# Kernel optimization log

Measured on AMD Instinct MI355X. Metric: run time of the kernel, lower is better.

## Reference

```python
import jax, jax.numpy as jnp
import numpy as np

S, M, B, D, H, DH = 1024, 1024, 4, 1024, 16, 64
T = S + M


def _rel_shift(x):
    # x: [i, j, b, n] -> Transformer-XL relative shift
    i, j = x.shape[0], x.shape[1]
    zero_pad = jnp.zeros((i, 1) + x.shape[2:], x.dtype)
    x_padded = jnp.concatenate([zero_pad, x], axis=1)
    x_padded = x_padded.reshape((j + 1, i) + x.shape[2:])
    return x_padded[1:].reshape(x.shape)


def setup_inputs() -> dict:
    key = jax.random.key(0)
    ks = jax.random.split(key, 8)
    sc = 0.02
    x = jax.random.normal(ks[0], (S, B, D), jnp.float32)
    memory = jax.random.normal(ks[1], (M, B, D), jnp.float32)
    pos_emb = jax.random.normal(ks[2], (T, D), jnp.float32)
    pos_bias_u = jax.random.normal(ks[3], (H, DH), jnp.float32) * sc
    pos_bias_v = jax.random.normal(ks[4], (H, DH), jnp.float32) * sc
    W_qkv = jax.random.normal(ks[5], (D, 3 * H * DH), jnp.float32) * sc
    W_rel = jax.random.normal(ks[6], (D, H * DH), jnp.float32) * sc
    W_o = jax.random.normal(ks[7], (H * DH, D), jnp.float32) * sc
    gamma = jnp.ones((D,), jnp.float32)
    beta = jnp.zeros((D,), jnp.float32)
    # causal mask accounting for memory: query i attends keys j <= i + M
    causal = jnp.arange(T)[None, :] > (jnp.arange(S)[:, None] + M)
    mask = jnp.broadcast_to(causal[:, :, None], (S, T, B))
    return {"x": x, "pos_emb": pos_emb, "pos_bias_u": pos_bias_u,
            "pos_bias_v": pos_bias_v, "memory": memory,
            "W_qkv": W_qkv, "W_rel": W_rel, "W_o": W_o,
            "gamma": gamma, "beta": beta, "mask": mask}


def reference(x, pos_emb, pos_bias_u, pos_bias_v, memory, W_qkv, W_rel, W_o, gamma, beta, mask):
    seq_len, batch, d_model = x.shape
    num_head, d_head = pos_bias_u.shape
    scale = 1.0 / d_head ** 0.5

    c = jnp.concatenate([memory, x], axis=0)          # [T, B, D]
    total_len = c.shape[0]

    qkv = c @ W_qkv                                   # [T, B, 3*H*DH]
    q, k, v = jnp.split(qkv, 3, axis=-1)
    q = q.reshape(total_len, batch, num_head, d_head)[-seq_len:]  # [S,B,H,DH]
    k = k.reshape(total_len, batch, num_head, d_head)             # [T,B,H,DH]
    v = v.reshape(total_len, batch, num_head, d_head)             # [T,B,H,DH]
    r = (pos_emb @ W_rel).reshape(total_len, num_head, d_head)    # [T,H,DH]

    AC = jnp.einsum('ibnd,jbnd->ijbn', q + pos_bias_u, k)  # content-content
    BD = jnp.einsum('ibnd,jnd->ijbn', q + pos_bias_v, r)   # content-position
    BD = _rel_shift(BD)

    attn_score = (AC + BD) * scale                    # [S,T,B,H]
    attn_score = jnp.where(mask[:, :, :, None], -jnp.inf, attn_score)
    attn_prob = jax.nn.softmax(attn_score, axis=1)

    attn_vec = jnp.einsum('ijbn,jbnd->ibnd', attn_prob, v)
    attn_vec = attn_vec.reshape(seq_len, batch, num_head * d_head)
    attn_out = attn_vec @ W_o                         # [S,B,D]

    y = x + attn_out
    mu = jnp.mean(y, axis=-1, keepdims=True)
    var = jnp.var(y, axis=-1, keepdims=True)
    return (y - mu) / jnp.sqrt(var + 1e-5) * gamma + beta
```

## Files before the change

kernel.cpp:

```cpp
#include <hip/hip_runtime.h>
#include <math.h>
#include <cstdint>
#include <cstddef>


typedef _Float16 half_t;
typedef _Float16 half8 __attribute__((ext_vector_type(8)));
typedef _Float16 half4v __attribute__((ext_vector_type(4)));
typedef float f32x4 __attribute__((ext_vector_type(4)));

#define S_LEN 1024
#define M_LEN 1024
#define T_LEN 2048
#define BATCH 4
#define NHEAD 16

__device__ inline void async_copy16(const half_t* g, half_t* l) {
  __builtin_amdgcn_global_load_lds(
      (const __attribute__((address_space(1))) void*)g,
      (__attribute__((address_space(3))) void*)l, 16, 0, 0);
}

__global__ __launch_bounds__(256) void k_convert3(const float* __restrict__ mem,
                                                  const float* __restrict__ x,
                                                  const float* __restrict__ pos,
                                                  half_t* __restrict__ cbf,
                                                  half_t* __restrict__ posb) {
  const int i = blockIdx.x * 256 + threadIdx.x;
  const float* src;
  half_t* dst;
  int off;
  if (i < 1048576)      { src = mem; dst = cbf;           off = i; }
  else if (i < 2097152) { src = x;   dst = cbf + 4194304; off = i - 1048576; }
  else                  { src = pos; dst = posb;          off = i - 2097152; }
  const float4 v = ((const float4*)src)[off];
  half4v h;
  h[0] = (half_t)v.x; h[1] = (half_t)v.y; h[2] = (half_t)v.z; h[3] = (half_t)v.w;
  ((half4v*)dst)[off] = h;
}

__global__ __launch_bounds__(256) void k_transpose_w3(const float* __restrict__ Wqkv,
                                                      const float* __restrict__ Wrel,
                                                      const float* __restrict__ Wo,
                                                      half_t* __restrict__ wqkvT,
                                                      half_t* __restrict__ wrelT,
                                                      half_t* __restrict__ woT) {
  __shared__ float tile[64][65];
  const int y = blockIdx.y;
  const float* src; half_t* dst; int C, c0;
  if (y < 48)      { src = Wqkv; dst = wqkvT; C = 3072; c0 = y * 64; }
  else if (y < 64) { src = Wrel; dst = wrelT; C = 1024; c0 = (y - 48) * 64; }
  else             { src = Wo;   dst = woT;   C = 1024; c0 = (y - 64) * 64; }
  const int t = threadIdx.x;
  const int r0 = blockIdx.x * 64;
  const int tx = t & 63, ty4 = t >> 6;
#pragma unroll
  for (int k = 0; k < 16; ++k) {
    int row = k * 4 + ty4;
    tile[row][tx] = src[(size_t)(r0 + row) * C + c0 + tx];
  }
  __syncthreads();
#pragma unroll
  for (int k = 0; k < 16; ++k) {
    int orow = k * 4 + ty4;
    dst[(size_t)(c0 + orow) * 1024 + r0 + tx] = (half_t)tile[tx][orow];
  }
}

__device__ inline void gemm_body(const half_t* __restrict__ A,
                                 const half_t* __restrict__ B,
                                 half_t* __restrict__ C,
                                 int N, int K, int ld, int m0, int n0,
                                 half_t (*ldsA)[64], half_t (*ldsB)[64]) {
  const int t = threadIdx.x;
  const int wave = t >> 6, lane = t & 63, quad = lane >> 4, l15 = lane & 15;
  const int wm = (wave >> 1) * 64, wn = (wave & 1) * 64;
  const int srow = lane >> 3;
  const int scol = ((lane & 7) ^ srow) * 8;
  f32x4 acc[4][4] = {};
  for (int k0 = 0; k0 < K; k0 += 64) {
    __syncthreads();
#pragma unroll
    for (int i = 0; i < 4; ++i) {
      const int r0 = (wave * 4 + i) * 8;
      async_copy16(&A[(size_t)(m0 + r0 + srow) * ld + k0 + scol], &ldsA[r0][0]);
      async_copy16(&B[(size_t)(n0 + r0 + srow) * ld + k0 + scol], &ldsB[r0][0]);
    }
    __syncthreads();
#pragma unroll
    for (int ks = 0; ks < 2; ++ks) {
      half8 af[4], bf[4];
#pragma unroll
      for (int mt = 0; mt < 4; ++mt)
        af[mt] = *(const half8*)&ldsA[wm + mt * 16 + l15][((ks * 4 + quad) ^ (l15 & 7)) * 8];
#pragma unroll
      for (int nt = 0; nt < 4; ++nt)
        bf[nt] = *(const half8*)&ldsB[wn + nt * 16 + l15][((ks * 4 + quad) ^ (l15 & 7)) * 8];
#pragma unroll
      for (int mt = 0; mt < 4; ++mt)
#pragma unroll
        for (int nt = 0; nt < 4; ++nt)
          acc[mt][nt] = __builtin_amdgcn_mfma_f32_16x16x32_f16(af[mt], bf[nt], acc[mt][nt], 0, 0, 0);
    }
  }
#pragma unroll
  for (int mt = 0; mt < 4; ++mt)
#pragma unroll
    for (int nt = 0; nt < 4; ++nt)
#pragma unroll
      for (int r = 0; r < 4; ++r) {
        const int row = m0 + wm + mt * 16 + quad * 4 + r;
        const int col = n0 + wn + nt * 16 + l15;
        C[(size_t)row * N + col] = (half_t)acc[mt][nt][r];
      }
}

#define QP_STAGE(buf_, k0_)                                                    \
  do {                                                                         \
    _Pragma("unroll") for (int i_ = 0; i_ < 4; ++i_) {                         \
      const int r0_ = wave * 32 + i_ * 8;                                      \
      async_copy16(&A[(size_t)(m0 + r0_ + srw) * 1024 + (k0_) + scl],          \
                   &ldsA[buf_][r0_][0]);                                       \
      async_copy16(&B[(size_t)(n0 + r0_ + srw) * 1024 + (k0_) + scl],          \
                   &ldsB[buf_][r0_][0]);                                       \
    }                                                                          \
  } while (0)

#define QP_COMPUTE(d_)                                                         \
  do {                                                                         \
    _Pragma("unroll") for (int ks_ = 0; ks_ < 2; ++ks_) {                      \
      half8 bf_[4];                                                            \
      _Pragma("unroll") for (int nt_ = 0; nt_ < 4; ++nt_) {                    \
        const int rw_ = wn + nt_ * 16 + l15;                                   \
        bf_[nt_] =                                                             \
            *(const half8*)&ldsB[d_][rw_][((ks_ * 4 + quad) ^ (rw_ & 7)) * 8]; \
      }                                                                        \
      half8 af_[8];                                                            \
      _Pragma("unroll") for (int mt_ = 0; mt_ < 8; ++mt_) {                    \
        const int rw_ = wm + mt_ * 16 + l15;                                   \
        af_[mt_] =                                                             \
            *(const half8*)&ldsA[d_][rw_][((ks_ * 4 + quad) ^ (rw_ & 7)) * 8]; \
      }                                                                        \
      __builtin_amdgcn_s_setprio(1);                                           \
      _Pragma("unroll") for (int mt_ = 0; mt_ < 8; ++mt_)                      \
        _Pragma("unroll") for (int nt_ = 0; nt_ < 4; ++nt_)                    \
          acc[mt_][nt_] = __builtin_amdgcn_mfma_f32_16x16x32_f16(              \
              af_[mt_], bf_[nt_], acc[mt_][nt_], 0, 0, 0);                     \
      __builtin_amdgcn_s_setprio(0);                                           \
    }                                                                          \
  } while (0)

__global__ __launch_bounds__(512, 2) void k_gemm_qkv_pos(const half_t* __restrict__ cbf,
                                                         const half_t* __restrict__ wqkvT,
                                                         half_t* __restrict__ qkv,
                                                         const half_t* __restrict__ posb,
                                                         const half_t* __restrict__ wrelT,
                                                         half_t* __restrict__ rb) {
  __shared__ half_t ldsA[2][256][64];
  __shared__ half_t ldsB[2][256][64];
  const int t = threadIdx.x;
  const int wave = t >> 6, lane = t & 63, quad = lane >> 4, l15 = lane & 15;
  const int bid0 = blockIdx.x;
  const int bid = (bid0 & 7) * 52 + (bid0 >> 3);
  const half_t* A; const half_t* B; half_t* C; int m0, n0, N;
  if (bid < 384) { A = cbf;  B = wqkvT; C = qkv; N = 3072;
                   m0 = (bid & 31) * 256; n0 = (bid >> 5) * 256; }
  else { const int b2 = bid - 384;
         A = posb; B = wrelT; C = rb;  N = 1024;
         m0 = (b2 & 7) * 256; n0 = (b2 >> 3) * 256; }
  const int srw = lane >> 3;
  const int scl = ((lane & 7) ^ srw) * 8;
  const int wm = (wave >> 2) * 128, wn = (wave & 3) * 64;

  f32x4 acc[8][4] = {};

  QP_STAGE(0, 0);
  __syncthreads();
  int d = 0;
  for (int kt = 0; kt < 15; ++kt) {
    QP_STAGE(d ^ 1, (kt + 1) * 64);
    QP_COMPUTE(d);
    __syncthreads();
    d ^= 1;
  }
  QP_COMPUTE(d);

#pragma unroll
  for (int mt = 0; mt < 8; ++mt)
#pragma unroll
    for (int nt = 0; nt < 4; ++nt)
#pragma unroll
      for (int r = 0; r < 4; ++r)
        C[(size_t)(m0 + wm + mt * 16 + quad * 4 + r) * N + n0 + wn + nt * 16 + l15] =
            (half_t)acc[mt][nt][r];
}

__global__ __launch_bounds__(256) void k_gemm_proj(const half_t* __restrict__ av,
                                                   const half_t* __restrict__ woT,
                                                   half_t* __restrict__ out0,
                                                   half_t* __restrict__ out1) {
  __shared__ half_t ldsA[128][64];
  __shared__ half_t ldsB[128][64];
  const int bid = blockIdx.x;
  const int h = bid >> 8, b2 = bid & 255;
  gemm_body(av + h * 512, woT + h * 512, h ? out1 : out0,
            1024, 512, 1024, (b2 & 31) * 128, (b2 >> 5) * 128, ldsA, ldsB);
}

__global__ __launch_bounds__(256) void k_transpose_v(const half_t* __restrict__ qkv,
                                                     half_t* __restrict__ vT) {
  __shared__ half_t tile[64][72];
  const int t = threadIdx.x;
  const int t0 = blockIdx.x * 64, bn = blockIdx.y, b = bn >> 4, n = bn & 15;
#pragma unroll
  for (int i = 0; i < 2; ++i) {
    const int ci = t + i * 256;
    const int row = ci >> 3, co = (ci & 7) * 8;
    *(half8*)&tile[row][co] =
        *(const half8*)&qkv[((size_t)(t0 + row) * BATCH + b) * 3072 + 2048 + n * 64 + co];
  }
  __syncthreads();
#pragma unroll
  for (int i = 0; i < 2; ++i) {
    const int ci = t + i * 256;
    const int dh = ci >> 3, to = (ci & 7) * 8;
    half8 v;
#pragma unroll
    for (int j = 0; j < 8; ++j) v[j] = tile[to + j][dh];
    *(half8*)&vT[((size_t)bn * 64 + dh) * 2048 + t0 + to] = v;
  }
}

__global__ __launch_bounds__(512, 4) void k_attn(const half_t* __restrict__ qkv,
                                                 const half_t* __restrict__ rbuf,
                                                 const half_t* __restrict__ vT,
                                                 const float* __restrict__ pbu,
                                                 const float* __restrict__ pbv,
                                                 half_t* __restrict__ av) {
  __shared__ __align__(16) half_t ldsK[64][64];
  __shared__ __align__(16) half_t ldsV[64][64];
  __shared__ __align__(16) half_t ldsR[256][64];
  __shared__ __align__(16) half_t ldsP[8][16][72];
  const int t = threadIdx.x;
  const int wave = t >> 6, lane = t & 63, quad = lane >> 4, l15 = lane & 15;

  const int li = blockIdx.x + 8 * blockIdx.y;
  const int c = li & 255, kr = li >> 8;
  const int xe = kr == 0 ? (c & 7) : 7 - (c & 7);
  const int bn = (c >> 3) + (kr << 5);
  const int i0 = xe * 128;
  const int b = bn >> 4, n = bn & 15;
  const int i_base = i0 + wave * 16;
  const int p0 = 896 - i0;

  half8 qu[2], qv[2];
#pragma unroll
  for (int ks = 0; ks < 2; ++ks) {
    const int dh0 = ks * 32 + quad * 8;
    const half8 qf = *(const half8*)&qkv[((size_t)(M_LEN + i_base + l15) * BATCH + b) * 3072 + n * 64 + dh0];
#pragma unroll
    for (int j = 0; j < 8; ++j) {
      const float qj = (float)qf[j];
      qu[ks][j] = (half_t)(qj + pbu[n * 64 + dh0 + j]);
      qv[ks][j] = (half_t)(qj + pbv[n * 64 + dh0 + j]);
    }
  }

  int bperm_idx[4];
  bool lo_sel[4];
#pragma unroll
  for (int r = 0; r < 4; ++r) {
    const int irow = quad * 4 + r;
    bperm_idx[r] = ((lane & 48) | ((l15 + 15 - irow) & 15)) << 2;
    lo_sel[r] = (l15 <= irow);
  }

  f32x4 oacc[4] = {};
  float lpart[4] = {0.f, 0.f, 0.f, 0.f};
  const float k1 = 0.125f * 1.44269504088896f;
  const float kC = -4.0f * 1.44269504088896f;

  const int srow = t >> 3, sc3 = t & 7;
  const int sxk = (sc3 ^ (srow & 7)) * 8;

  const int ntile = xe * 2 + 18;

  half8 kreg = *(const half8*)&qkv[((size_t)srow * BATCH + b) * 3072 + 1024 + n * 64 + sc3 * 8];
  half8 vreg = *(const half8*)&vT[((size_t)bn * 64 + srow) * 2048 + sc3 * 8];
  half8 rreg4[4];
  int rr4[4], rc4[4];
#pragma unroll
  for (int i = 0; i < 4; ++i) {
    const int ci = t + 512 * i;
    rr4[i] = ci >> 3; rc4[i] = ci & 7;
    const int ps = p0 + rr4[i] > 2047 ? 2047 : p0 + rr4[i];
    rreg4[i] = *(const half8*)&rbuf[(size_t)ps * 1024 + n * 64 + rc4[i] * 8];
  }
  half8 rpre;

  for (int kt = 0; kt < ntile; ++kt) {
    const int j0 = kt * 64;

    __syncthreads();
    *(half8*)&ldsK[srow][sxk] = kreg;
    *(half8*)&ldsV[srow][sxk] = vreg;
    if (kt == 0) {
#pragma unroll
      for (int i = 0; i < 4; ++i) {
        const int pg = p0 + rr4[i];
        *(half8*)&ldsR[pg & 255][(rc4[i] ^ (pg & 7)) * 8] = rreg4[i];
      }
    } else {
      const int pw = j0 + p0 + 192 + srow;
      *(half8*)&ldsR[pw & 255][(sc3 ^ (pw & 7)) * 8] = rpre;
    }
    __syncthreads();

    if (kt + 1 < ntile) {
      const int j0n = j0 + 64;
      kreg = *(const half8*)&qkv[((size_t)(j0n + srow) * BATCH + b) * 3072 + 1024 + n * 64 + sc3 * 8];
      vreg = *(const half8*)&vT[((size_t)bn * 64 + srow) * 2048 + j0n + sc3 * 8];
      const int pn = j0 + p0 + 256 + srow;
      const int pc = pn > 2047 ? 2047 : pn;
      rpre = *(const half8*)&rbuf[(size_t)pc * 1024 + n * 64 + sc3 * 8];
    }

    f32x4 ac[4] = {};
#pragma unroll
    for (int ks = 0; ks < 2; ++ks)
#pragma unroll
      for (int nt = 0; nt < 4; ++nt) {
        const int row = nt * 16 + l15;
        const half8 kf = *(const half8*)&ldsK[row][((ks * 4 + quad) ^ (row & 7)) * 8];
        ac[nt] = __builtin_amdgcn_mfma_f32_16x16x32_f16(qu[ks], kf, ac[nt], 0, 0, 0);
      }

    const int rbg = j0 + p0 + 112 - wave * 16;
    f32x4 ea[5] = {};
#pragma unroll
    for (int ks = 0; ks < 2; ++ks)
#pragma unroll
      for (int et = 0; et < 5; ++et) {
        const int pr = rbg + et * 16 + l15;
        const half8 rf = *(const half8*)&ldsR[pr & 255][((ks * 4 + quad) ^ (pr & 7)) * 8];
        ea[et] = __builtin_amdgcn_mfma_f32_16x16x32_f16(qv[ks], rf, ea[et], 0, 0, 0);
      }

    const bool maskt = j0 > i_base + 960;
#pragma unroll
    for (int r = 0; r < 4; ++r) {
      const int irow = quad * 4 + r;
      const int ig = i_base + irow;
      float rot[5];
#pragma unroll
      for (int et = 0; et < 5; ++et)
        rot[et] = __int_as_float(
            __builtin_amdgcn_ds_bpermute(bperm_idx[r], __float_as_int(ea[et][r])));
      float psum = 0.f;
#pragma unroll
      for (int nt = 0; nt < 4; ++nt) {
        const float ev = lo_sel[r] ? rot[nt] : rot[nt + 1];
        const int cj = nt * 16 + l15;
        float p = __builtin_amdgcn_exp2f(fmaf(ac[nt][r] + ev, k1, kC));
        if (maskt && (j0 + cj > ig + M_LEN)) p = 0.f;
        psum += p;
        ldsP[wave][irow][cj] = (half_t)p;
      }
      lpart[r] += psum;
    }
    __builtin_amdgcn_wave_barrier();

    half8 pa[2];
#pragma unroll
    for (int ks = 0; ks < 2; ++ks)
      pa[ks] = *(const half8*)&ldsP[wave][l15][ks * 32 + quad * 8];
#pragma unroll
    for (int ks = 0; ks < 2; ++ks)
#pragma unroll
      for (int dnt = 0; dnt < 4; ++dnt) {
        const int row = dnt * 16 + l15;
        const half8 vf = *(const half8*)&ldsV[row][((ks * 4 + quad) ^ (row & 7)) * 8];
        oacc[dnt] = __builtin_amdgcn_mfma_f32_16x16x32_f16(pa[ks], vf, oacc[dnt], 0, 0, 0);
      }
  }

#pragma unroll
  for (int r = 0; r < 4; ++r) {
    float l = lpart[r];
#pragma unroll
    for (int off = 1; off < 16; off <<= 1) l += __shfl_xor(l, off);
    const float inv = 1.0f / l;
    const int ig = i_base + quad * 4 + r;
#pragma unroll
    for (int dnt = 0; dnt < 4; ++dnt)
      av[((size_t)ig * BATCH + b) * 1024 + n * 64 + dnt * 16 + l15] = (half_t)(oacc[dnt][r] * inv);
  }
}

__global__ __launch_bounds__(256) void k_ln(const float* __restrict__ x,
                                            const half_t* __restrict__ ao0,
                                            const half_t* __restrict__ ao1,
                                            const float* __restrict__ gamma,
                                            const float* __restrict__ beta,
                                            float* __restrict__ out) {
  const int row = blockIdx.x;
  const int t = threadIdx.x;
  const float4 xv = ((const float4*)(x + (size_t)row * 1024))[t];
  const half4v a4 = ((const half4v*)(ao0 + (size_t)row * 1024))[t];
  const half4v b4 = ((const half4v*)(ao1 + (size_t)row * 1024))[t];
  const float y0 = xv.x + (float)a4[0] + (float)b4[0];
  const float y1 = xv.y + (float)a4[1] + (float)b4[1];
  const float y2 = xv.z + (float)a4[2] + (float)b4[2];
  const float y3 = xv.w + (float)a4[3] + (float)b4[3];
  float s = y0 + y1 + y2 + y3;
  float ss = y0 * y0 + y1 * y1 + y2 * y2 + y3 * y3;
#pragma unroll
  for (int off = 1; off < 64; off <<= 1) {
    s += __shfl_xor(s, off);
    ss += __shfl_xor(ss, off);
  }
  __shared__ float sb[4], ssb[4];
  if ((t & 63) == 0) { sb[t >> 6] = s; ssb[t >> 6] = ss; }
  __syncthreads();
  s = sb[0] + sb[1] + sb[2] + sb[3];
  ss = ssb[0] + ssb[1] + ssb[2] + ssb[3];
  const float mean = s * (1.f / 1024.f);
  const float var = ss * (1.f / 1024.f) - mean * mean;
  const float rstd = rsqrtf(var + 1e-5f);
  const float4 g = ((const float4*)gamma)[t];
  const float4 be = ((const float4*)beta)[t];
  float4 o;
  o.x = (y0 - mean) * rstd * g.x + be.x;
  o.y = (y1 - mean) * rstd * g.y + be.y;
  o.z = (y2 - mean) * rstd * g.z + be.z;
  o.w = (y3 - mean) * rstd * g.w + be.w;
  ((float4*)(out + (size_t)row * 1024))[t] = o;
}

extern "C" void kernel_launch(void* const* d_in, const int* in_sizes, int n_in,
                              void* d_out, int out_size, void* d_ws, size_t ws_size,
                              hipStream_t stream) {
  const float* x     = (const float*)d_in[0];
  const float* pos   = (const float*)d_in[1];
  const float* pbu   = (const float*)d_in[2];
  const float* pbv   = (const float*)d_in[3];
  const float* mem   = (const float*)d_in[4];
  const float* Wqkv  = (const float*)d_in[5];
  const float* Wrel  = (const float*)d_in[6];
  const float* Wo    = (const float*)d_in[7];
  const float* gamma = (const float*)d_in[8];
  const float* beta  = (const float*)d_in[9];
  float* out = (float*)d_out;

  half_t* ws    = (half_t*)d_ws;
  half_t* cbf   = ws;
  half_t* posb  = cbf + 8388608;
  half_t* wqkvT = posb + 2097152;
  half_t* wrelT = wqkvT + 3145728;
  half_t* woT   = wrelT + 1048576;
  half_t* qkv   = woT + 1048576;
  half_t* rb    = qkv + 25165824;
  half_t* vT    = rb + 2097152;
  half_t* av    = vT + 8388608;
  half_t* aout0 = qkv;
  half_t* aout1 = qkv + 4194304;

  k_convert3<<<10240, 256, 0, stream>>>(mem, x, pos, cbf, posb);
  k_transpose_w3<<<dim3(16, 80), 256, 0, stream>>>(Wqkv, Wrel, Wo, wqkvT, wrelT, woT);
  k_gemm_qkv_pos<<<416, 512, 0, stream>>>(cbf, wqkvT, qkv, posb, wrelT, rb);
  k_transpose_v<<<dim3(32, 64), 256, 0, stream>>>(qkv, vT);
  k_attn<<<dim3(8, 64), 512, 0, stream>>>(qkv, rb, vT, pbu, pbv, av);
  k_gemm_proj<<<512, 256, 0, stream>>>(av, woT, aout0, aout1);
  k_ln<<<4096, 256, 0, stream>>>(x, aout0, aout1, gamma, beta, out);
}
```

Measured before the change: 330.5 us.

## Compute V transposed directly in GEMM, fuse prep kernels, reorder rows batch-major

Merges the input-conversion and weight-transpose kernels into a single launch. The conversion now writes the concatenated activations batch-major. The QKV GEMM is split so that Q/K go to a narrower buffer. V is produced already transposed by swapping the operands (W_v^T times activations), which removes the separate V-transpose kernel and its round trip through memory. The attention kernel's indexing is updated for the new layouts. The cost is that the V-part blocks write with a large stride (N=8192), and one fewer launch boundary is traded for a more branchy prep kernel.

```diff
diff --git a/kernel.cpp b/kernel.cpp
--- a/kernel.cpp
+++ b/kernel.cpp
@@ -21,38 +21,47 @@
       (__attribute__((address_space(3))) void*)l, 16, 0, 0);
 }
 
-__global__ __launch_bounds__(256) void k_convert3(const float* __restrict__ mem,
-                                                  const float* __restrict__ x,
-                                                  const float* __restrict__ pos,
-                                                  half_t* __restrict__ cbf,
-                                                  half_t* __restrict__ posb) {
-  const int i = blockIdx.x * 256 + threadIdx.x;
-  const float* src;
-  half_t* dst;
-  int off;
-  if (i < 1048576)      { src = mem; dst = cbf;           off = i; }
-  else if (i < 2097152) { src = x;   dst = cbf + 4194304; off = i - 1048576; }
-  else                  { src = pos; dst = posb;          off = i - 2097152; }
-  const float4 v = ((const float4*)src)[off];
-  half4v h;
-  h[0] = (half_t)v.x; h[1] = (half_t)v.y; h[2] = (half_t)v.z; h[3] = (half_t)v.w;
-  ((half4v*)dst)[off] = h;
-}
-
-__global__ __launch_bounds__(256) void k_transpose_w3(const float* __restrict__ Wqkv,
-                                                      const float* __restrict__ Wrel,
-                                                      const float* __restrict__ Wo,
-                                                      half_t* __restrict__ wqkvT,
-                                                      half_t* __restrict__ wrelT,
-                                                      half_t* __restrict__ woT) {
+__global__ __launch_bounds__(256) void k_pre(const float* __restrict__ mem,
+                                             const float* __restrict__ x,
+                                             const float* __restrict__ pos,
+                                             const float* __restrict__ Wqkv,
+                                             const float* __restrict__ Wrel,
+                                             const float* __restrict__ Wo,
+                                             half_t* __restrict__ cbf,
+                                             half_t* __restrict__ posb,
+                                             half_t* __restrict__ wqkvT,
+                                             half_t* __restrict__ wrelT,
+                                             half_t* __restrict__ woT) {
   __shared__ float tile[64][65];
-  const int y = blockIdx.y;
+  const int bid = blockIdx.x;
+  const int t = threadIdx.x;
+  if (bid < 10240) {
+    const int i = bid * 256 + t;
+    if (i < 2097152) {
+      const int off = i & 1048575;
+      const int sel = i >> 20;
+      const float4 v = ((const float4*)(sel ? x : mem))[off];
+      const int row = off >> 8, d4 = off & 255;
+      const int drow = (row & 3) * 2048 + sel * 1024 + (row >> 2);
+      half4v h;
+      h[0] = (half_t)v.x; h[1] = (half_t)v.y; h[2] = (half_t)v.z; h[3] = (half_t)v.w;
+      ((half4v*)cbf)[(drow << 8) + d4] = h;
+    } else {
+      const int off = i - 2097152;
+      const float4 v = ((const float4*)pos)[off];
+      half4v h;
+      h[0] = (half_t)v.x; h[1] = (half_t)v.y; h[2] = (half_t)v.z; h[3] = (half_t)v.w;
+      ((half4v*)posb)[off] = h;
+    }
+    return;
+  }
+  const int tb = bid - 10240;
+  const int bx = tb & 15, y = tb >> 4;
   const float* src; half_t* dst; int C, c0;
   if (y < 48)      { src = Wqkv; dst = wqkvT; C = 3072; c0 = y * 64; }
   else if (y < 64) { src = Wrel; dst = wrelT; C = 1024; c0 = (y - 48) * 64; }
   else             { src = Wo;   dst = woT;   C = 1024; c0 = (y - 64) * 64; }
-  const int t = threadIdx.x;
-  const int r0 = blockIdx.x * 64;
+  const int r0 = bx * 64;
   const int tx = t & 63, ty4 = t >> 6;
 #pragma unroll
   for (int k = 0; k < 16; ++k) {
@@ -155,7 +164,8 @@
                                                          half_t* __restrict__ qkv,
                                                          const half_t* __restrict__ posb,
                                                          const half_t* __restrict__ wrelT,
-                                                         half_t* __restrict__ rb) {
+                                                         half_t* __restrict__ rb,
+                                                         half_t* __restrict__ vT) {
   __shared__ half_t ldsA[2][256][64];
   __shared__ half_t ldsB[2][256][64];
   const int t = threadIdx.x;
@@ -163,11 +173,18 @@
   const int bid0 = blockIdx.x;
   const int bid = (bid0 & 7) * 52 + (bid0 >> 3);
   const half_t* A; const half_t* B; half_t* C; int m0, n0, N;
-  if (bid < 384) { A = cbf;  B = wqkvT; C = qkv; N = 3072;
-                   m0 = (bid & 31) * 256; n0 = (bid >> 5) * 256; }
-  else { const int b2 = bid - 384;
-         A = posb; B = wrelT; C = rb;  N = 1024;
-         m0 = (b2 & 7) * 256; n0 = (b2 >> 3) * 256; }
+  if (bid < 256) {
+    A = cbf;  B = wqkvT; C = qkv; N = 2048;
+    m0 = (bid & 31) * 256; n0 = (bid >> 5) * 256;
+  } else if (bid < 384) {
+    const int b2 = bid - 256;
+    A = wqkvT + 2048 * 1024; B = cbf; C = vT; N = 8192;
+    m0 = (b2 & 3) * 256; n0 = (b2 >> 2) * 256;
+  } else {
+    const int b2 = bid - 384;
+    A = posb; B = wrelT; C = rb; N = 1024;
+    m0 = (b2 & 7) * 256; n0 = (b2 >> 3) * 256;
+  }
   const int srw = lane >> 3;
   const int scl = ((lane & 7) ^ srw) * 8;
   const int wm = (wave >> 2) * 128, wn = (wave & 3) * 64;
@@ -205,30 +222,6 @@
   const int h = bid >> 8, b2 = bid & 255;
   gemm_body(av + h * 512, woT + h * 512, h ? out1 : out0,
             1024, 512, 1024, (b2 & 31) * 128, (b2 >> 5) * 128, ldsA, ldsB);
-}
-
-__global__ __launch_bounds__(256) void k_transpose_v(const half_t* __restrict__ qkv,
-                                                     half_t* __restrict__ vT) {
-  __shared__ half_t tile[64][72];
-  const int t = threadIdx.x;
-  const int t0 = blockIdx.x * 64, bn = blockIdx.y, b = bn >> 4, n = bn & 15;
-#pragma unroll
-  for (int i = 0; i < 2; ++i) {
-    const int ci = t + i * 256;
-    const int row = ci >> 3, co = (ci & 7) * 8;
-    *(half8*)&tile[row][co] =
-        *(const half8*)&qkv[((size_t)(t0 + row) * BATCH + b) * 3072 + 2048 + n * 64 + co];
-  }
-  __syncthreads();
-#pragma unroll
-  for (int i = 0; i < 2; ++i) {
-    const int ci = t + i * 256;
-    const int dh = ci >> 3, to = (ci & 7) * 8;
-    half8 v;
-#pragma unroll
-    for (int j = 0; j < 8; ++j) v[j] = tile[to + j][dh];
-    *(half8*)&vT[((size_t)bn * 64 + dh) * 2048 + t0 + to] = v;
-  }
 }
 
 __global__ __launch_bounds__(512, 4) void k_attn(const half_t* __restrict__ qkv,
@@ -257,7 +250,7 @@
 #pragma unroll
   for (int ks = 0; ks < 2; ++ks) {
     const int dh0 = ks * 32 + quad * 8;
-    const half8 qf = *(const half8*)&qkv[((size_t)(M_LEN + i_base + l15) * BATCH + b) * 3072 + n * 64 + dh0];
+    const half8 qf = *(const half8*)&qkv[((size_t)(b * 2048 + M_LEN + i_base + l15)) * 2048 + n * 64 + dh0];
 #pragma unroll
     for (int j = 0; j < 8; ++j) {
       const float qj = (float)qf[j];
@@ -285,8 +278,8 @@
 
   const int ntile = xe * 2 + 18;
 
-  half8 kreg = *(const half8*)&qkv[((size_t)srow * BATCH + b) * 3072 + 1024 + n * 64 + sc3 * 8];
-  half8 vreg = *(const half8*)&vT[((size_t)bn * 64 + srow) * 2048 + sc3 * 8];
+  half8 kreg = *(const half8*)&qkv[((size_t)(b * 2048 + srow)) * 2048 + 1024 + n * 64 + sc3 * 8];
+  half8 vreg = *(const half8*)&vT[((size_t)(n * 64 + srow)) * 8192 + b * 2048 + sc3 * 8];
   half8 rreg4[4];
   int rr4[4], rc4[4];
 #pragma unroll
@@ -318,8 +311,8 @@
 
     if (kt + 1 < ntile) {
       const int j0n = j0 + 64;
-      kreg = *(const half8*)&qkv[((size_t)(j0n + srow) * BATCH + b) * 3072 + 1024 + n * 64 + sc3 * 8];
-      vreg = *(const half8*)&vT[((size_t)bn * 64 + srow) * 2048 + j0n + sc3 * 8];
+      kreg = *(const half8*)&qkv[((size_t)(b * 2048 + j0n + srow)) * 2048 + 1024 + n * 64 + sc3 * 8];
+      vreg = *(const half8*)&vT[((size_t)(n * 64 + srow)) * 8192 + b * 2048 + j0n + sc3 * 8];
       const int pn = j0 + p0 + 256 + srow;
       const int pc = pn > 2047 ? 2047 : pn;
       rpre = *(const half8*)&rbuf[(size_t)pc * 1024 + n * 64 + sc3 * 8];
@@ -459,16 +452,14 @@
   half_t* wrelT = wqkvT + 3145728;
   half_t* woT   = wrelT + 1048576;
   half_t* qkv   = woT + 1048576;
-  half_t* rb    = qkv + 25165824;
+  half_t* rb    = qkv + 16777216;
   half_t* vT    = rb + 2097152;
   half_t* av    = vT + 8388608;
   half_t* aout0 = qkv;
   half_t* aout1 = qkv + 4194304;
 
-  k_convert3<<<10240, 256, 0, stream>>>(mem, x, pos, cbf, posb);
-  k_transpose_w3<<<dim3(16, 80), 256, 0, stream>>>(Wqkv, Wrel, Wo, wqkvT, wrelT, woT);
-  k_gemm_qkv_pos<<<416, 512, 0, stream>>>(cbf, wqkvT, qkv, posb, wrelT, rb);
-  k_transpose_v<<<dim3(32, 64), 256, 0, stream>>>(qkv, vT);
+  k_pre<<<11520, 256, 0, stream>>>(mem, x, pos, Wqkv, Wrel, Wo, cbf, posb, wqkvT, wrelT, woT);
+  k_gemm_qkv_pos<<<416, 512, 0, stream>>>(cbf, wqkvT, qkv, posb, wrelT, rb, vT);
   k_attn<<<dim3(8, 64), 512, 0, stream>>>(qkv, rb, vT, pbu, pbv, av);
   k_gemm_proj<<<512, 256, 0, stream>>>(av, woT, aout0, aout1);
   k_ln<<<4096, 256, 0, stream>>>(x, aout0, aout1, gamma, beta, out);
```

After: 308.4 us. -6.7%, faster.
